# Kernel tuning notes

Measured on AMD Instinct MI355X. Metric: run time of the kernel, lower is better.

## Reference

```python
import jax, jax.numpy as jnp
import numpy as np

B, NE, NI, D = 256, 1024, 1024, 256  # batch, E cells, I cells, patch dim (16x16)
K_GAIN, N_EXP = 0.04, 2.0            # power-law i/o: k * relu(I)**n
TAU_E, TAU_I, DT = 0.02, 0.01, 0.001
STEPS, LAST_N = 200, 50              # int(T/dt) with T=0.2; average last 50 states
S_EE0, S_EI0, S_IE0, S_II0 = 3.75, 1.86, 3.13, 1.11 - 0.02
EPS = 1e-12
JEE, JEI, JIE, JII = 0.044, 0.023, 0.042, 0.018
SIGMA = 32.0


def ring_kernel(n_post, n_pre, sigma=SIGMA):
    post = np.linspace(0.0, 180.0, n_post + 1)[:-1]
    pre = np.linspace(0.0, 180.0, n_pre + 1)[:-1]
    d = np.abs(post[:, None] - pre[None, :])
    d = np.minimum(d, 180.0 - d)
    return np.exp(-(d * d) / (2.0 * sigma * sigma)).astype(np.float32)


def setup_inputs() -> dict:
    key = jax.random.key(0)
    kx, kE, kI = jax.random.split(key, 3)
    x_batch = jax.random.uniform(kx, (B, D), dtype=jnp.float32)
    W_EE = JEE * ring_kernel(NE, NE)
    np.fill_diagonal(W_EE, 0.0)
    W_EI = JEI * ring_kernel(NE, NI)
    W_IE = JIE * ring_kernel(NI, NE)
    W_II = JII * ring_kernel(NI, NI)
    np.fill_diagonal(W_II, 0.0)
    Wff_E = 0.1 * jax.random.uniform(kE, (NE, D), dtype=jnp.float32)
    Wff_E = Wff_E / (jnp.linalg.norm(Wff_E, axis=1, keepdims=True) + 1e-8)
    Wff_I = 0.1 * jax.random.uniform(kI, (NI, D), dtype=jnp.float32)
    Wff_I = Wff_I / (jnp.linalg.norm(Wff_I, axis=1, keepdims=True) + 1e-8)
    return {
        'x_batch': x_batch,
        'W_EE': jnp.asarray(W_EE), 'W_EI': jnp.asarray(W_EI),
        'W_IE': jnp.asarray(W_IE), 'W_II': jnp.asarray(W_II),
        'Wff_E': Wff_E, 'Wff_I': Wff_I,
    }


def powerlaw_io(I):
    return K_GAIN * jnp.maximum(I, 0.0) ** N_EXP


def reference(x_batch, W_EE, W_EI, W_IE, W_II, Wff_E, Wff_I):
    # per-postsynaptic current scalers (computed under no_grad in torch)
    gE_E = jax.lax.stop_gradient(S_EE0 / (W_EE.sum(axis=1) + EPS))
    gI_E = jax.lax.stop_gradient(S_EI0 / (W_EI.sum(axis=1) + EPS))
    gE_I = jax.lax.stop_gradient(S_IE0 / (W_IE.sum(axis=1) + EPS))
    gI_I = jax.lax.stop_gradient(S_II0 / (W_II.sum(axis=1) + EPS))
    # in-place clamp + rescale of weights (as in forward_dynamics)
    W_EE = jnp.minimum(W_EE, 0.15) * gE_E[:, None]
    W_EI = jnp.maximum(W_EI, 0.0005) * gI_E[:, None]
    W_IE = W_IE * gE_I[:, None]
    W_II = W_II * gI_I[:, None]

    Iff_E = x_batch @ Wff_E.T  # (B, nE)
    Iff_I = x_batch @ Wff_I.T  # (B, nI)

    def step(carry, t):
        rE, rI, accE, accI = carry
        IE = Iff_E + rE @ W_EE.T - rI @ W_EI.T
        II = Iff_I + rE @ W_IE.T - rI @ W_II.T
        rE = rE + (DT / TAU_E) * (-rE + powerlaw_io(IE))
        rI = rI + (DT / TAU_I) * (-rI + powerlaw_io(II))
        w = (t >= STEPS - LAST_N).astype(rE.dtype)
        return (rE, rI, accE + w * rE, accI + w * rI), None

    z = jnp.zeros((B, NE), dtype=x_batch.dtype)
    zi = jnp.zeros((B, NI), dtype=x_batch.dtype)
    (rE, rI, accE, accI), _ = jax.lax.scan(step, (z, zi, z, zi), jnp.arange(STEPS))
    rE_bar = accE / LAST_N
    rI_bar = accI / LAST_N
    return (rE_bar, rI_bar)
```

## Files before the change

kernel.cpp:

```cpp
#include <hip/hip_runtime.h>
#include <stdint.h>

typedef __attribute__((ext_vector_type(8))) _Float16 f16x8;
typedef __attribute__((ext_vector_type(8))) unsigned short u16x8;
typedef __attribute__((ext_vector_type(4))) float f32x4;

__device__ __forceinline__ float bf2f(unsigned short u) {
    union { uint32_t u; float f; } v; v.u = ((uint32_t)u) << 16; return v.f;
}
__device__ __forceinline__ unsigned short f2h(float f) {
    _Float16 h = (_Float16)f;
    return __builtin_bit_cast(unsigned short, h);
}
__device__ __forceinline__ f32x4 MFMAH(u16x8 a, u16x8 b, f32x4 c) {
    return __builtin_amdgcn_mfma_f32_16x16x32_f16(
        __builtin_bit_cast(f16x8, a), __builtin_bit_cast(f16x8, b), c, 0, 0, 0);
}

__device__ __forceinline__ int is_f32(const void* p) {
    const uint32_t* u = (const uint32_t*)p;
    int c = 0;
    #pragma unroll
    for (int i = 0; i < 64; i++) c += (u[i] >> 15) & 1;
    return c >= 4;
}
__device__ __forceinline__ float load_any(const void* base, size_t idx, int f32) {
    return f32 ? ((const float*)base)[idx] : bf2f(((const unsigned short*)base)[idx]);
}

__global__ void zero_kernel(float* __restrict__ p) {
    p[(size_t)blockIdx.x * 256 + threadIdx.x] = 0.0f;
}

__global__ void conv_kernel(const void* __restrict__ src, unsigned short* __restrict__ dst,
                            int clamp_wei) {
    int f32 = is_f32(src);
    size_t base = ((size_t)blockIdx.x * 256 + threadIdx.x) * 8;
    unsigned short v[8];
    if (f32) {
        const float* s = (const float*)src + base;
        #pragma unroll
        for (int e = 0; e < 8; e++) {
            float f = s[e];
            if (clamp_wei) f = fmaxf(f, 0.0005f);
            v[e] = f2h(f);
        }
    } else {
        const unsigned short* s = (const unsigned short*)src + base;
        #pragma unroll
        for (int e = 0; e < 8; e++) {
            float f = bf2f(s[e]);
            if (clamp_wei) f = fmaxf(f, 0.0005f);
            v[e] = f2h(f);
        }
    }
    *(u16x8*)(dst + base) = *(u16x8*)v;
}

__global__ void g_kernel(const void* __restrict__ WEE, const void* __restrict__ WEI,
                         const void* __restrict__ WIE, const void* __restrict__ WII,
                         float* __restrict__ gE, float* __restrict__ gI) {
    int i = blockIdx.x;
    int tid = threadIdx.x;
    const void* TE; const void* TI; float sEc, sIc; size_t row;
    if (i < 1024) { TE = WEE; TI = WEI; sEc = 3.75f; sIc = 1.86f; row = i; }
    else          { TE = WIE; TI = WII; sEc = 3.13f; sIc = (float)(1.11 - 0.02); row = i - 1024; }
    int fE = is_f32(TE), fI = is_f32(TI);
    float se = 0.f, si = 0.f;
    for (int j = tid; j < 1024; j += 256) {
        se += load_any(TE, row * 1024 + j, fE);
        si += load_any(TI, row * 1024 + j, fI);
    }
    for (int o = 32; o > 0; o >>= 1) { se += __shfl_down(se, o); si += __shfl_down(si, o); }
    __shared__ float lsE[4], lsI[4];
    int w = tid >> 6;
    if ((tid & 63) == 0) { lsE[w] = se; lsI[w] = si; }
    __syncthreads();
    if (tid == 0) {
        float te = lsE[0] + lsE[1] + lsE[2] + lsE[3];
        float ti = lsI[0] + lsI[1] + lsI[2] + lsI[3];
        gE[i] = sEc / (te + 1e-12f);
        gI[i] = sIc / (ti + 1e-12f);
    }
}

__global__ __launch_bounds__(256) void iff_kernel(const unsigned short* __restrict__ x,
                                                  const unsigned short* __restrict__ WffE,
                                                  const unsigned short* __restrict__ WffI,
                                                  float* __restrict__ Iff) {
    int n0 = blockIdx.x * 32;
    int m0 = blockIdx.y * 64;
    int tid = threadIdx.x, w = tid >> 6, lane = tid & 63;
    int l15 = lane & 15, quad = lane >> 4;
    int arow = m0 + 16 * w + l15;
    int nA = n0 + l15, nB = n0 + 16 + l15;
    const unsigned short* bA = (nA < 1024) ? (WffE + (size_t)nA * 256) : (WffI + (size_t)(nA - 1024) * 256);
    const unsigned short* bB = (nB < 1024) ? (WffE + (size_t)nB * 256) : (WffI + (size_t)(nB - 1024) * 256);
    f32x4 acc0 = {0.f, 0.f, 0.f, 0.f}, acc1 = {0.f, 0.f, 0.f, 0.f};
    #pragma unroll
    for (int ks = 0; ks < 8; ks++) {
        int k = ks * 32 + quad * 8;
        u16x8 a  = *(const u16x8*)(x + (size_t)arow * 256 + k);
        u16x8 b0 = *(const u16x8*)(bA + k);
        u16x8 b1 = *(const u16x8*)(bB + k);
        acc0 = MFMAH(a, b0, acc0);
        acc1 = MFMAH(a, b1, acc1);
    }
    #pragma unroll
    for (int v = 0; v < 4; v++) {
        int row = m0 + 16 * w + quad * 4 + v;
        Iff[(size_t)row * 2048 + n0 + l15]      = acc0[v];
        Iff[(size_t)row * 2048 + n0 + 16 + l15] = acc1[v];
    }
}

#define FLAG_STRIDE 32
__global__ __launch_bounds__(1024, 4) void persist_kernel(
    const unsigned short* __restrict__ WEEc, const unsigned short* __restrict__ WEIc,
    const unsigned short* __restrict__ WIEc, const unsigned short* __restrict__ WIIc,
    unsigned short* __restrict__ h0, unsigned short* __restrict__ h1,
    const float* __restrict__ Iff, const float* __restrict__ gE, const float* __restrict__ gI,
    float* __restrict__ out, int* __restrict__ flags)
{
    __shared__ unsigned short Wl[32 * 2048];
    __shared__ f32x4 PA[12 * 64];
    __shared__ f32x4 PB[12 * 64];

    int bid = blockIdx.x;
    int nT = bid & 63;
    int mT = bid >> 6;
    int n0 = nT * 32;
    int m0 = mT * 64;
    int tid = threadIdx.x;
    int wave = tid >> 6, lane = tid & 63;
    int w = wave & 3;
    int wq = wave >> 2;
    int l15 = lane & 15, quad = lane >> 4;

    bool isEblk = (n0 < 1024);
    const unsigned short* W0 = isEblk ? WEEc : WIEc;
    const unsigned short* W1 = isEblk ? WEIc : WIIc;
    int nbase = n0 & 1023;

    {
        int c = tid & 255;
        int r0 = tid >> 8;
        int k = c * 8;
        const unsigned short* s0 = W0 + (size_t)nbase * 1024;
        const unsigned short* s1 = W1 + (size_t)nbase * 1024;
        #pragma unroll
        for (int i = 0; i < 8; i++) {
            int row = r0 * 8 + i;
            const unsigned short* src = (k < 1024) ? (s0 + (size_t)row * 1024 + k)
                                                   : (s1 + (size_t)row * 1024 + (k - 1024));
            int gs = (c + row) & 255;
            *(u16x8*)(Wl + row * 2048 + gs * 8) = *(const u16x8*)src;
        }
    }
    __syncthreads();

    int arow = m0 + 16 * w + l15;
    int colA = n0 + l15, colB = colA + 16;
    float invtau = isEblk ? 0.05f : 0.1f;
    bool ehalf = (wq < 2);
    float sgA = ehalf ? gE[colA] : -gI[colA];
    float sgB = ehalf ? gE[colB] : -gI[colB];

    float iffA[4], iffB[4], rstA[4], rstB[4], sumA[4], sumB[4];
    int orow[4];
    if (wq == 0) {
        #pragma unroll
        for (int v = 0; v < 4; v++) {
            orow[v] = m0 + 16 * w + quad * 4 + v;
            iffA[v] = Iff[(size_t)orow[v] * 2048 + colA];
            iffB[v] = Iff[(size_t)orow[v] * 2048 + colB];
            rstA[v] = 0.f; rstB[v] = 0.f; sumA[v] = 0.f; sumB[v] = 0.f;
        }
    }

    const unsigned short* hi_in = h0;
    unsigned short* hi_out = h1;
    const unsigned short* WlA = Wl + l15 * 2048;
    const unsigned short* WlB = Wl + (16 + l15) * 2048;
    int slot = ((wq - 1) << 2) | w;

    for (int t = 0; t < 200; t++) {
        const unsigned short* hp = hi_in + (size_t)arow * 2048 + wq * 512;

        f32x4 cA0 = {0,0,0,0}, cA1 = {0,0,0,0}, cB0 = {0,0,0,0}, cB1 = {0,0,0,0};
        #pragma unroll 8
        for (int i = 0; i < 16; i++) {
            int k = i * 32 + quad * 8;
            int g = 4 * (wq * 16 + i) + quad;
            u16x8 a  = *(const u16x8*)(hp + k);
            u16x8 b0 = *(const u16x8*)(WlA + ((g + l15) & 255) * 8);
            u16x8 b1 = *(const u16x8*)(WlB + ((g + l15 + 16) & 255) * 8);
            if (i & 1) { cA1 = MFMAH(a, b0, cA1); cB1 = MFMAH(a, b1, cB1); }
            else       { cA0 = MFMAH(a, b0, cA0); cB0 = MFMAH(a, b1, cB0); }
        }
        f32x4 pA = sgA * (cA0 + cA1);
        f32x4 pB = sgB * (cB0 + cB1);

        if (wq != 0) {
            PA[slot * 64 + lane] = pA;
            PB[slot * 64 + lane] = pB;
        }
        __syncthreads();

        if (wq == 0) {
            f32x4 tA = pA + PA[w * 64 + lane] + PA[(4 + w) * 64 + lane] + PA[(8 + w) * 64 + lane];
            f32x4 tB = pB + PB[w * 64 + lane] + PB[(4 + w) * 64 + lane] + PB[(8 + w) * 64 + lane];
            float wacc = (t >= 150) ? 1.0f : 0.0f;
            #pragma unroll
            for (int v = 0; v < 4; v++) {
                size_t idx = (size_t)orow[v] * 2048;
                {
                    float I = iffA[v] + tA[v];
                    float rl = fmaxf(I, 0.f);
                    float rnew = rstA[v] + invtau * (0.04f * rl * rl - rstA[v]);
                    rstA[v] = rnew;
                    __hip_atomic_store(hi_out + idx + colA, f2h(rnew),
                                       __ATOMIC_RELAXED, __HIP_MEMORY_SCOPE_AGENT);
                    sumA[v] += wacc * rnew;
                }
                {
                    float I = iffB[v] + tB[v];
                    float rl = fmaxf(I, 0.f);
                    float rnew = rstB[v] + invtau * (0.04f * rl * rl - rstB[v]);
                    rstB[v] = rnew;
                    __hip_atomic_store(hi_out + idx + colB, f2h(rnew),
                                       __ATOMIC_RELAXED, __HIP_MEMORY_SCOPE_AGENT);
                    sumB[v] += wacc * rnew;
                }
            }
        }
        if (t == 199) break;

        __syncthreads();
        if (tid == 0) {
            __hip_atomic_store(&flags[bid * FLAG_STRIDE], t + 1,
                               __ATOMIC_RELAXED, __HIP_MEMORY_SCOPE_AGENT);
        }
        if (tid < 64) {
            const int fi = (mT * 64 + tid) * FLAG_STRIDE;
            while (__hip_atomic_load(&flags[fi], __ATOMIC_RELAXED,
                                     __HIP_MEMORY_SCOPE_AGENT) < t + 1) {
                __builtin_amdgcn_s_sleep(1);
            }
        }
        __syncthreads();
        if (tid == 0) {
            __builtin_amdgcn_fence(__ATOMIC_ACQUIRE, "agent");
        }
        __syncthreads();

        const unsigned short* th = hi_in; hi_in = hi_out; hi_out = (unsigned short*)th;
    }

    if (wq == 0) {
        float* ob = out + (isEblk ? 0 : 262144);
        #pragma unroll
        for (int v = 0; v < 4; v++) {
            ob[(size_t)orow[v] * 1024 + nbase + l15]      = sumA[v] * (1.0f / 50.0f);
            ob[(size_t)orow[v] * 1024 + nbase + 16 + l15] = sumB[v] * (1.0f / 50.0f);
        }
    }
}

extern "C" void kernel_launch(void* const* d_in, const int* in_sizes, int n_in,
                              void* d_out, int out_size, void* d_ws, size_t ws_size,
                              hipStream_t stream) {
    const void* x    = d_in[0];
    const void* WEE  = d_in[1];
    const void* WEI  = d_in[2];
    const void* WIE  = d_in[3];
    const void* WII  = d_in[4];
    const void* WffE = d_in[5];
    const void* WffI = d_in[6];

    char* ws = (char*)d_ws;
    const size_t MB = 1024 * 1024;
    const size_t KB = 1024;
    unsigned short* h0    = (unsigned short*)(ws + 0);
    int*            flags = (int*)(ws + 1 * MB);
    unsigned short* h1    = (unsigned short*)(ws + 2 * MB);
    float*          Iff   = (float*)(ws + 3 * MB);
    unsigned short* WEEc  = (unsigned short*)(ws + 5 * MB);
    unsigned short* WEIc  = (unsigned short*)(ws + 7 * MB);
    unsigned short* WIEc  = (unsigned short*)(ws + 9 * MB);
    unsigned short* WIIc  = (unsigned short*)(ws + 11 * MB);
    unsigned short* xc    = (unsigned short*)(ws + 13 * MB);
    unsigned short* WffEc = (unsigned short*)(ws + 13 * MB + 128 * KB);
    unsigned short* WffIc = (unsigned short*)(ws + 13 * MB + 640 * KB);
    float*          gE    = (float*)(ws + 13 * MB + 1152 * KB);
    float*          gI    = gE + 2048;

    zero_kernel<<<1056, 256, 0, stream>>>((float*)ws);

    conv_kernel<<<32,  256, 0, stream>>>(x,    xc,    0);
    conv_kernel<<<512, 256, 0, stream>>>(WEE,  WEEc,  0);
    conv_kernel<<<512, 256, 0, stream>>>(WEI,  WEIc,  1);
    conv_kernel<<<512, 256, 0, stream>>>(WIE,  WIEc,  0);
    conv_kernel<<<512, 256, 0, stream>>>(WII,  WIIc,  0);
    conv_kernel<<<128, 256, 0, stream>>>(WffE, WffEc, 0);
    conv_kernel<<<128, 256, 0, stream>>>(WffI, WffIc, 0);

    g_kernel<<<2048, 256, 0, stream>>>(WEE, WEI, WIE, WII, gE, gI);
    iff_kernel<<<dim3(64, 4), 256, 0, stream>>>(xc, WffEc, WffIc, Iff);

    float* outp = (float*)d_out;
    void* args[] = { &WEEc, &WEIc, &WIEc, &WIIc, &h0, &h1,
                     &Iff, &gE, &gI, &outp, &flags };
    hipLaunchCooperativeKernel((const void*)persist_kernel, dim3(256), dim3(1024),
                               args, 0, stream);
}
```

Before: 2.223 ms.

## Use per-wave packed flags for grid barrier and preload hidden-state fragments

The per-block flag barrier is replaced by per-wave flags packed contiguously per row-tile. Each output wave publishes its own flag right after its stores drain, and a single wave polls all 256 flags with four vector loads, which removes one __syncthreads and the padded flag stride. The MFMA loop is also fully unrolled, with 12 of its 16 A fragments loaded up front to hide global load latency. This raises register pressure, and its correctness relies on s_waitcnt ordering the stores before the flag write, plus the flag array layout changing consistently with any host-side reset.

```diff
diff --git a/kernel.cpp b/kernel.cpp
--- a/kernel.cpp
+++ b/kernel.cpp
@@ -114,7 +114,6 @@
     }
 }
 
-#define FLAG_STRIDE 32
 __global__ __launch_bounds__(1024, 4) void persist_kernel(
     const unsigned short* __restrict__ WEEc, const unsigned short* __restrict__ WEIc,
     const unsigned short* __restrict__ WIEc, const unsigned short* __restrict__ WIIc,
@@ -183,20 +182,25 @@
     const unsigned short* WlA = Wl + l15 * 2048;
     const unsigned short* WlB = Wl + (16 + l15) * 2048;
     int slot = ((wq - 1) << 2) | w;
+    const int fbase = mT * 256;
 
     for (int t = 0; t < 200; t++) {
         const unsigned short* hp = hi_in + (size_t)arow * 2048 + wq * 512;
 
+        u16x8 a[12];
+        #pragma unroll
+        for (int i = 0; i < 12; i++)
+            a[i] = *(const u16x8*)(hp + i * 32 + quad * 8);
+
         f32x4 cA0 = {0,0,0,0}, cA1 = {0,0,0,0}, cB0 = {0,0,0,0}, cB1 = {0,0,0,0};
-        #pragma unroll 8
+        #pragma unroll
         for (int i = 0; i < 16; i++) {
-            int k = i * 32 + quad * 8;
+            u16x8 av = (i < 12) ? a[i] : *(const u16x8*)(hp + i * 32 + quad * 8);
             int g = 4 * (wq * 16 + i) + quad;
-            u16x8 a  = *(const u16x8*)(hp + k);
             u16x8 b0 = *(const u16x8*)(WlA + ((g + l15) & 255) * 8);
             u16x8 b1 = *(const u16x8*)(WlB + ((g + l15 + 16) & 255) * 8);
-            if (i & 1) { cA1 = MFMAH(a, b0, cA1); cB1 = MFMAH(a, b1, cB1); }
-            else       { cA0 = MFMAH(a, b0, cA0); cB0 = MFMAH(a, b1, cB0); }
+            if (i & 1) { cA1 = MFMAH(av, b0, cA1); cB1 = MFMAH(av, b1, cB1); }
+            else       { cA0 = MFMAH(av, b0, cA0); cB0 = MFMAH(av, b1, cB0); }
         }
         f32x4 pA = sgA * (cA0 + cA1);
         f32x4 pB = sgB * (cB0 + cB1);
@@ -233,18 +237,21 @@
                     sumB[v] += wacc * rnew;
                 }
             }
+            if (t != 199 && lane == 0) {
+                asm volatile("s_waitcnt vmcnt(0)" ::: "memory");
+                __hip_atomic_store(&flags[fbase + w * 64 + nT], t + 1,
+                                   __ATOMIC_RELAXED, __HIP_MEMORY_SCOPE_AGENT);
+            }
         }
         if (t == 199) break;
 
-        __syncthreads();
-        if (tid == 0) {
-            __hip_atomic_store(&flags[bid * FLAG_STRIDE], t + 1,
-                               __ATOMIC_RELAXED, __HIP_MEMORY_SCOPE_AGENT);
-        }
-        if (tid < 64) {
-            const int fi = (mT * 64 + tid) * FLAG_STRIDE;
-            while (__hip_atomic_load(&flags[fi], __ATOMIC_RELAXED,
-                                     __HIP_MEMORY_SCOPE_AGENT) < t + 1) {
+        if (wave == 4) {
+            while (true) {
+                int f0 = __hip_atomic_load(&flags[fbase + lane],       __ATOMIC_RELAXED, __HIP_MEMORY_SCOPE_AGENT);
+                int f1 = __hip_atomic_load(&flags[fbase + 64 + lane],  __ATOMIC_RELAXED, __HIP_MEMORY_SCOPE_AGENT);
+                int f2 = __hip_atomic_load(&flags[fbase + 128 + lane], __ATOMIC_RELAXED, __HIP_MEMORY_SCOPE_AGENT);
+                int f3 = __hip_atomic_load(&flags[fbase + 192 + lane], __ATOMIC_RELAXED, __HIP_MEMORY_SCOPE_AGENT);
+                if (f0 >= t + 1 && f1 >= t + 1 && f2 >= t + 1 && f3 >= t + 1) break;
                 __builtin_amdgcn_s_sleep(1);
             }
         }
```

Measured after the change: 3.328 ms. 49.7% more time.

## Stage new rates in LDS, publish coalesced 8-byte stores, split flag signaling from polling

Applied to the files above, without the earlier changes.

New f16 rates are first written to a shared tile, then copied to global memory as coalesced 8-byte atomic stores by 512 threads instead of scattered 2-byte atomic stores. An intra-block counter makes sure all waves' stores have completed before the block's flag is set. A separate wave polls the other blocks' flags and skips its own, so signaling and waiting can overlap. This adds an LDS round trip and a workgroup spin counter, and relies on s_waitcnt ordering before the relaxed flag store for correctness.

```diff
diff --git a/kernel.cpp b/kernel.cpp
--- a/kernel.cpp
+++ b/kernel.cpp
@@ -125,6 +125,8 @@
     __shared__ unsigned short Wl[32 * 2048];
     __shared__ f32x4 PA[12 * 64];
     __shared__ f32x4 PB[12 * 64];
+    __shared__ unsigned short Hs[64 * 32];
+    __shared__ int sbar;
 
     int bid = blockIdx.x;
     int nT = bid & 63;
@@ -143,6 +145,7 @@
     int nbase = n0 & 1023;
 
     {
+        if (tid == 0) sbar = 0;
         int c = tid & 255;
         int r0 = tid >> 8;
         int k = c * 8;
@@ -183,6 +186,8 @@
     const unsigned short* WlA = Wl + l15 * 2048;
     const unsigned short* WlB = Wl + (16 + l15) * 2048;
     int slot = ((wq - 1) << 2) | w;
+    int srow = tid >> 3;
+    int sc4  = (tid & 7) * 4;
 
     for (int t = 0; t < 200; t++) {
         const unsigned short* hp = hi_in + (size_t)arow * 2048 + wq * 512;
@@ -213,14 +218,13 @@
             float wacc = (t >= 150) ? 1.0f : 0.0f;
             #pragma unroll
             for (int v = 0; v < 4; v++) {
-                size_t idx = (size_t)orow[v] * 2048;
+                int r = 16 * w + quad * 4 + v;
                 {
                     float I = iffA[v] + tA[v];
                     float rl = fmaxf(I, 0.f);
                     float rnew = rstA[v] + invtau * (0.04f * rl * rl - rstA[v]);
                     rstA[v] = rnew;
-                    __hip_atomic_store(hi_out + idx + colA, f2h(rnew),
-                                       __ATOMIC_RELAXED, __HIP_MEMORY_SCOPE_AGENT);
+                    Hs[r * 32 + l15] = f2h(rnew);
                     sumA[v] += wacc * rnew;
                 }
                 {
@@ -228,8 +232,7 @@
                     float rl = fmaxf(I, 0.f);
                     float rnew = rstB[v] + invtau * (0.04f * rl * rl - rstB[v]);
                     rstB[v] = rnew;
-                    __hip_atomic_store(hi_out + idx + colB, f2h(rnew),
-                                       __ATOMIC_RELAXED, __HIP_MEMORY_SCOPE_AGENT);
+                    Hs[r * 32 + 16 + l15] = f2h(rnew);
                     sumB[v] += wacc * rnew;
                 }
             }
@@ -237,14 +240,30 @@
         if (t == 199) break;
 
         __syncthreads();
-        if (tid == 0) {
-            __hip_atomic_store(&flags[bid * FLAG_STRIDE], t + 1,
-                               __ATOMIC_RELAXED, __HIP_MEMORY_SCOPE_AGENT);
-        }
-        if (tid < 64) {
-            const int fi = (mT * 64 + tid) * FLAG_STRIDE;
-            while (__hip_atomic_load(&flags[fi], __ATOMIC_RELAXED,
-                                     __HIP_MEMORY_SCOPE_AGENT) < t + 1) {
+
+        if (tid < 512) {
+            unsigned long long pv = *(const unsigned long long*)(Hs + srow * 32 + sc4);
+            __hip_atomic_store((unsigned long long*)(hi_out + (size_t)(m0 + srow) * 2048 + n0 + sc4),
+                               pv, __ATOMIC_RELAXED, __HIP_MEMORY_SCOPE_AGENT);
+            asm volatile("s_waitcnt vmcnt(0)" ::: "memory");
+            if ((tid & 63) == 0) atomicAdd(&sbar, 1);
+            if (tid == 0) {
+                while (__hip_atomic_load(&sbar, __ATOMIC_RELAXED,
+                                         __HIP_MEMORY_SCOPE_WORKGROUP) < 8) {
+                    __builtin_amdgcn_s_sleep(1);
+                }
+                __hip_atomic_store(&flags[bid * FLAG_STRIDE], t + 1,
+                                   __ATOMIC_RELAXED, __HIP_MEMORY_SCOPE_AGENT);
+                sbar = 0;
+            }
+        } else if (wave == 15) {
+            const int fi = (mT * 64 + lane) * FLAG_STRIDE;
+            int self = (lane == nT);
+            while (true) {
+                int f = self ? (t + 1)
+                             : __hip_atomic_load(&flags[fi], __ATOMIC_RELAXED,
+                                                 __HIP_MEMORY_SCOPE_AGENT);
+                if (__all(f >= t + 1)) break;
                 __builtin_amdgcn_s_sleep(1);
             }
         }
```

Result: slower. 2.339 ms (+5.2%).
